# Kernel optimization log

Hardware: AMD Instinct MI355X
Metric: run time of the kernel (lower is better)

Reference implementation:

```python
import jax, jax.numpy as jnp
import numpy as np

N, E, F_IN, H, G, C = 50000, 600000, 128, 128, 500, 10


def _lin(k, fi, fo):
    # Glorot-ish scaled init for a [fi, fo] weight
    return (jax.random.normal(k, (fi, fo), jnp.float32) / np.float32(np.sqrt(fi)))


def setup_inputs() -> dict:
    key = jax.random.key(0)
    ks = jax.random.split(key, 16)
    x = jax.random.normal(ks[0], (N, F_IN), jnp.float32)
    edge_index = jax.random.randint(ks[1], (2, E), 0, N, dtype=jnp.int32)
    batch = jnp.sort(jax.random.randint(ks[2], (N,), 0, G, dtype=jnp.int32))
    return {
        "x": x, "edge_index": edge_index, "batch": batch,
        # SAGEConv i: out = mean_aggr @ Wl + bl + x @ Wr  (PyG default: mean aggr, root weight, bias on lin_l)
        "Wl1": _lin(ks[3], F_IN, H), "bl1": jnp.zeros((H,), jnp.float32), "Wr1": _lin(ks[4], F_IN, H),
        "Wl2": _lin(ks[5], H, H),    "bl2": jnp.zeros((H,), jnp.float32), "Wr2": _lin(ks[6], H, H),
        "Wl3": _lin(ks[7], H, H),    "bl3": jnp.zeros((H,), jnp.float32), "Wr3": _lin(ks[8], H, H),
        "W4": _lin(ks[9], H, 64), "b4": jnp.zeros((64,), jnp.float32),
        "W5": _lin(ks[10], 64, C), "b5": jnp.zeros((C,), jnp.float32),
    }


def _segment_mean(vals, ids, num_segments):
    s = jax.ops.segment_sum(vals, ids, num_segments=num_segments)
    cnt = jax.ops.segment_sum(jnp.ones((vals.shape[0], 1), vals.dtype), ids, num_segments=num_segments)
    return s / jnp.maximum(cnt, 1.0)


def _sage_conv(x, src, dst, Wl, bl, Wr):
    # gather source features along edges, mean-aggregate at destinations
    aggr = _segment_mean(x[src], dst, N)  # [N, F]
    return aggr @ Wl + bl + x @ Wr


def reference(x, edge_index, batch, Wl1, bl1, Wr1, Wl2, bl2, Wr2, Wl3, bl3, Wr3, W4, b4, W5, b5):
    src, dst = edge_index[0], edge_index[1]
    h = jax.nn.relu(_sage_conv(x, src, dst, Wl1, bl1, Wr1))
    h = jax.nn.relu(_sage_conv(h, src, dst, Wl2, bl2, Wr2))
    h = jax.nn.relu(_sage_conv(h, src, dst, Wl3, bl3, Wr3))
    g = _segment_mean(h, batch, G)          # global mean pool -> [G, H]
    g = jax.nn.relu(g @ W4 + b4)
    return jax.nn.log_softmax(g @ W5 + b5, axis=-1)
```

## Files before the change

### kernel.cpp

```cpp
#include <hip/hip_runtime.h>
#include <hip/hip_bf16.h>
#include <math.h>

#define FH 128

typedef __attribute__((ext_vector_type(8))) short short8v;
typedef __attribute__((ext_vector_type(4))) float float4v;
typedef unsigned short ushort_t;
typedef unsigned int   uint32;

__device__ __forceinline__ ushort_t f2bf(float f) {
    uint32 u = __builtin_bit_cast(uint32, f);
    u += 0x7fffu + ((u >> 16) & 1u);
    return (ushort_t)(u >> 16);
}
__device__ __forceinline__ float bf_lo(uint32 w) { return __builtin_bit_cast(float, w << 16); }
__device__ __forceinline__ float bf_hi(uint32 w) { return __builtin_bit_cast(float, w & 0xffff0000u); }
__device__ __forceinline__ uint32 pack2(float lo, float hi) {
    return (uint32)f2bf(lo) | ((uint32)f2bf(hi) << 16);
}

__global__ __launch_bounds__(256) void zero_kernel(int* __restrict__ p, int n) {
    int i = (blockIdx.x * 256 + threadIdx.x) * 4;
    if (i + 3 < n) {
        *(int4*)(p + i) = make_int4(0, 0, 0, 0);
    } else {
        for (int j = i; j < n; ++j) p[j] = 0;
    }
}

__device__ __forceinline__ void pack_one(const float* __restrict__ Wl,
                                         const float* __restrict__ Wr,
                                         ushort_t* __restrict__ Bp, int t) {
    int k = t >> 7, n = t & 127;
    float v = (k < FH) ? Wl[k * FH + n] : Wr[(k - FH) * FH + n];
    int nt = n >> 4, kt = k >> 5;
    int lane = (n & 15) + (((k >> 3) & 3) << 4);
    int j = k & 7;
    Bp[(((nt * 8 + kt) * 64) + lane) * 8 + j] = f2bf(v);
}

__global__ __launch_bounds__(256) void fused_prep_kernel(
        const float* __restrict__ x, ushort_t* __restrict__ xb, size_t n, int cvtBlocks,
        const float* __restrict__ Wl1, const float* __restrict__ Wr1, ushort_t* __restrict__ Bp1,
        const float* __restrict__ Wl2, const float* __restrict__ Wr2, ushort_t* __restrict__ Bp2,
        const float* __restrict__ Wl3, const float* __restrict__ Wr3, ushort_t* __restrict__ Bp3,
        const int* __restrict__ dst, int* __restrict__ deg, int E, int degBlocks,
        const int* __restrict__ batch, int* __restrict__ gstart, int N, int G) {
    int b = blockIdx.x;
    if (b < cvtBlocks) {
        size_t base = ((size_t)b * 256 + threadIdx.x) * 8;
        if (base >= n) return;
        const float4 a = *(const float4*)(x + base);
        const float4 c = *(const float4*)(x + base + 4);
        ushort_t o[8] = {f2bf(a.x), f2bf(a.y), f2bf(a.z), f2bf(a.w),
                         f2bf(c.x), f2bf(c.y), f2bf(c.z), f2bf(c.w)};
        *(uint4*)(xb + base) = *(const uint4*)o;
        return;
    }
    b -= cvtBlocks;
    if (b < 384) {
        int which = b >> 7;
        int t = (b & 127) * 256 + threadIdx.x;
        if (which == 0)      pack_one(Wl1, Wr1, Bp1, t);
        else if (which == 1) pack_one(Wl2, Wr2, Bp2, t);
        else                 pack_one(Wl3, Wr3, Bp3, t);
        return;
    }
    b -= 384;
    if (b < degBlocks) {
        int e = b * 256 + threadIdx.x;
        if (e < E) atomicAdd(&deg[dst[e]], 1);
        return;
    }
    b -= degBlocks;
    {
        int g = b * 256 + threadIdx.x;
        if (g > G) return;
        int lo = 0, hi = N;
        while (lo < hi) {
            int mid = (lo + hi) >> 1;
            if (batch[mid] < g) lo = mid + 1; else hi = mid;
        }
        gstart[g] = lo;
    }
}

__global__ __launch_bounds__(256) void scan1_kernel(const int* __restrict__ deg,
                                                    int* __restrict__ rowptr,
                                                    int* __restrict__ blockSums, int N) {
    __shared__ int lds[256];
    const int base = blockIdx.x * 1024;
    const int t = threadIdx.x;
    int v[4]; int sum = 0;
    #pragma unroll
    for (int j = 0; j < 4; ++j) {
        int idx = base + t * 4 + j;
        v[j] = (idx < N) ? deg[idx] : 0;
        sum += v[j];
    }
    lds[t] = sum; __syncthreads();
    for (int off = 1; off < 256; off <<= 1) {
        int val = lds[t];
        int add = (t >= off) ? lds[t - off] : 0;
        __syncthreads();
        lds[t] = val + add;
        __syncthreads();
    }
    int run = (t > 0) ? lds[t - 1] : 0;
    #pragma unroll
    for (int j = 0; j < 4; ++j) {
        int idx = base + t * 4 + j;
        if (idx < N) rowptr[idx] = run;
        run += v[j];
    }
    if (t == 255) blockSums[blockIdx.x] = lds[255];
}

__global__ __launch_bounds__(256) void scan3_kernel(int* __restrict__ rowptr,
                                                    int* __restrict__ pos,
                                                    const int* __restrict__ blockSums,
                                                    int N, int nb) {
    __shared__ int sAdd, sTot;
    if (threadIdx.x < 64) {
        const int lane = threadIdx.x;
        const int bid = blockIdx.x;
        int pre = 0, tot = 0;
        for (int i = lane; i < nb; i += 64) {
            const int v = blockSums[i];
            tot += v;
            if (i < bid) pre += v;
        }
        #pragma unroll
        for (int off = 1; off < 64; off <<= 1) {
            pre += __shfl_xor(pre, off);
            tot += __shfl_xor(tot, off);
        }
        if (lane == 0) { sAdd = pre; sTot = tot; }
    }
    __syncthreads();
    const int add = sAdd;
    const int base = blockIdx.x * 1024;
    #pragma unroll
    for (int j = 0; j < 4; ++j) {
        int idx = base + threadIdx.x * 4 + j;
        if (idx < N) {
            int v = rowptr[idx] + add;
            rowptr[idx] = v;
            pos[idx] = v;
        }
    }
    if (blockIdx.x == (unsigned)(nb - 1) && threadIdx.x == 0) rowptr[N] = sTot;
}

__global__ __launch_bounds__(256) void fill_csr_kernel(const int* __restrict__ src,
                                                       const int* __restrict__ dst,
                                                       int* __restrict__ pos,
                                                       int* __restrict__ csr, int E) {
    int e = blockIdx.x * 256 + threadIdx.x;
    if (e >= E) return;
    int idx = atomicAdd(&pos[dst[e]], 1);
    csr[idx] = src[e];
}

__global__ __launch_bounds__(256) void pull_mean_kernel(const ushort_t* __restrict__ x,
                                                        const int* __restrict__ rowptr,
                                                        const int* __restrict__ csr,
                                                        ushort_t* __restrict__ aggr, int N) {
    const int v = (blockIdx.x * 256 + threadIdx.x) >> 6;
    if (v >= N) return;
    const int lane = threadIdx.x & 63;
    const int grp  = lane >> 4;
    const int li   = lane & 15;
    const int beg = rowptr[v], end = rowptr[v + 1];
    const uint4* xp = (const uint4*)x + li;

    const uint4 z = {0u, 0u, 0u, 0u};
    uint4 w0 = z, w1 = z, w2 = z, w3 = z;
    const int i0 = beg + grp;
    if (i0 < end)      w0 = xp[(size_t)csr[i0] * 16];
    if (i0 + 4 < end)  w1 = xp[(size_t)csr[i0 + 4] * 16];
    if (i0 + 8 < end)  w2 = xp[(size_t)csr[i0 + 8] * 16];
    if (i0 + 12 < end) w3 = xp[(size_t)csr[i0 + 12] * 16];

    float a0 = (bf_lo(w0.x) + bf_lo(w1.x)) + (bf_lo(w2.x) + bf_lo(w3.x));
    float a1 = (bf_hi(w0.x) + bf_hi(w1.x)) + (bf_hi(w2.x) + bf_hi(w3.x));
    float a2 = (bf_lo(w0.y) + bf_lo(w1.y)) + (bf_lo(w2.y) + bf_lo(w3.y));
    float a3 = (bf_hi(w0.y) + bf_hi(w1.y)) + (bf_hi(w2.y) + bf_hi(w3.y));
    float a4 = (bf_lo(w0.z) + bf_lo(w1.z)) + (bf_lo(w2.z) + bf_lo(w3.z));
    float a5 = (bf_hi(w0.z) + bf_hi(w1.z)) + (bf_hi(w2.z) + bf_hi(w3.z));
    float a6 = (bf_lo(w0.w) + bf_lo(w1.w)) + (bf_lo(w2.w) + bf_lo(w3.w));
    float a7 = (bf_hi(w0.w) + bf_hi(w1.w)) + (bf_hi(w2.w) + bf_hi(w3.w));

    for (int i = beg + 16 + grp; i < end; i += 4) {
        const uint4 w = xp[(size_t)csr[i] * 16];
        a0 += bf_lo(w.x); a1 += bf_hi(w.x); a2 += bf_lo(w.y); a3 += bf_hi(w.y);
        a4 += bf_lo(w.z); a5 += bf_hi(w.z); a6 += bf_lo(w.w); a7 += bf_hi(w.w);
    }

    a0 += __shfl_xor(a0, 16); a1 += __shfl_xor(a1, 16);
    a2 += __shfl_xor(a2, 16); a3 += __shfl_xor(a3, 16);
    a4 += __shfl_xor(a4, 16); a5 += __shfl_xor(a5, 16);
    a6 += __shfl_xor(a6, 16); a7 += __shfl_xor(a7, 16);
    a0 += __shfl_xor(a0, 32); a1 += __shfl_xor(a1, 32);
    a2 += __shfl_xor(a2, 32); a3 += __shfl_xor(a3, 32);
    a4 += __shfl_xor(a4, 32); a5 += __shfl_xor(a5, 32);
    a6 += __shfl_xor(a6, 32); a7 += __shfl_xor(a7, 32);

    if (grp == 0) {
        const float inv = 1.0f / (float)max(end - beg, 1);
        uint4 o;
        o.x = pack2(a0 * inv, a1 * inv);
        o.y = pack2(a2 * inv, a3 * inv);
        o.z = pack2(a4 * inv, a5 * inv);
        o.w = pack2(a6 * inv, a7 * inv);
        ((uint4*)aggr)[(size_t)v * 16 + li] = o;
    }
}

#define SO_STRIDE 136
__global__ __launch_bounds__(256) void sage_mfma_kernel(const ushort_t* __restrict__ xin,
                                                        const ushort_t* __restrict__ aggr,
                                                        const ushort_t* __restrict__ Bp,
                                                        const float* __restrict__ bl,
                                                        ushort_t* __restrict__ out, int M) {
    __shared__ ushort_t sB[16384];
    const int tid = threadIdx.x;
    const int wave = tid >> 6;
    const int lane = tid & 63;
    const int grp  = lane >> 4;
    const int li   = lane & 15;
    const int rowBase = (blockIdx.x * 4 + wave) * 16;
    const int arow = min(rowBase + li, M - 1);

    short8v afrag[8];
    #pragma unroll
    for (int kt = 0; kt < 4; ++kt)
        afrag[kt] = *(const short8v*)(aggr + (size_t)arow * FH + kt * 32 + grp * 8);
    #pragma unroll
    for (int kt = 0; kt < 4; ++kt)
        afrag[4 + kt] = *(const short8v*)(xin + (size_t)arow * FH + kt * 32 + grp * 8);

    float4v acc[8];
    #pragma unroll
    for (int ch = 0; ch < 2; ++ch) {
        if (ch) __syncthreads();
        {
            const uint4* s = (const uint4*)Bp + ch * 2048;
            uint4* d = (uint4*)sB;
            #pragma unroll
            for (int i = 0; i < 8; ++i)
                d[tid + 256 * i] = s[tid + 256 * i];
        }
        __syncthreads();
        #pragma unroll
        for (int ntl = 0; ntl < 4; ++ntl) {
            const int nt = ch * 4 + ntl;
            acc[nt] = (float4v){0.f, 0.f, 0.f, 0.f};
            #pragma unroll
            for (int kt = 0; kt < 8; ++kt) {
                const short8v b = *(const short8v*)(sB + (((ntl * 8 + kt) * 64) + lane) * 8);
                acc[nt] = __builtin_amdgcn_mfma_f32_16x16x32_bf16(afrag[kt], b, acc[nt], 0, 0, 0);
            }
        }
    }

    __syncthreads();

    ushort_t* so = sB + wave * (16 * SO_STRIDE);
    #pragma unroll
    for (int nt = 0; nt < 8; ++nt) {
        const float bias = bl[nt * 16 + li];
        #pragma unroll
        for (int r = 0; r < 4; ++r)
            so[(grp * 4 + r) * SO_STRIDE + nt * 16 + li] = f2bf(fmaxf(acc[nt][r] + bias, 0.f));
    }
    #pragma unroll
    for (int t = 0; t < 4; ++t) {
        const int idx = lane + 64 * t;
        const int r  = idx >> 4;
        const int ch = idx & 15;
        const int row = rowBase + r;
        if (row < M) {
            const uint4 val = *(const uint4*)(so + r * SO_STRIDE + ch * 8);
            *(uint4*)(out + (size_t)row * FH + ch * 8) = val;
        }
    }
}

__global__ __launch_bounds__(256) void head_kernel(const ushort_t* __restrict__ h,
                                                   const int* __restrict__ gstart,
                                                   const float* __restrict__ W4,
                                                   const float* __restrict__ b4,
                                                   const float* __restrict__ W5,
                                                   const float* __restrict__ b5,
                                                   float* __restrict__ out, int G) {
    __shared__ float sred[4][FH];
    __shared__ float sg2[64];
    __shared__ float sl[10];
    __shared__ float slse;
    const int g = blockIdx.x;
    const int t = threadIdx.x;
    const int wave = t >> 6, lane = t & 63;
    const int beg = gstart[g], end = gstart[g + 1];

    const uint32* hp = (const uint32*)h + lane;
    float a0 = 0.f, a1 = 0.f;
    for (int i = beg + wave; i < end; i += 4) {
        const uint32 w = hp[(size_t)i * 64];
        a0 += bf_lo(w); a1 += bf_hi(w);
    }
    sred[wave][lane * 2]     = a0;
    sred[wave][lane * 2 + 1] = a1;
    __syncthreads();
    if (t < FH) {
        const float s = sred[0][t] + sred[1][t] + sred[2][t] + sred[3][t];
        sred[0][t] = s / (float)max(end - beg, 1);
    }
    __syncthreads();
    if (t < 64) {
        float acc = b4[t];
        #pragma unroll 4
        for (int k = 0; k < FH; ++k)
            acc += sred[0][k] * W4[k * 64 + t];
        sg2[t] = fmaxf(acc, 0.f);
    }
    __syncthreads();
    if (t < 10) {
        float acc = b5[t];
        #pragma unroll 4
        for (int k = 0; k < 64; ++k)
            acc += sg2[k] * W5[k * 10 + t];
        sl[t] = acc;
    }
    __syncthreads();
    if (t == 0) {
        float m = sl[0];
        #pragma unroll
        for (int j = 1; j < 10; ++j) m = fmaxf(m, sl[j]);
        float s = 0.f;
        #pragma unroll
        for (int j = 0; j < 10; ++j) s += expf(sl[j] - m);
        slse = m + logf(s);
    }
    __syncthreads();
    if (t < 10) out[g * 10 + t] = sl[t] - slse;
}

extern "C" void kernel_launch(void* const* d_in, const int* in_sizes, int n_in,
                              void* d_out, int out_size, void* d_ws, size_t ws_size,
                              hipStream_t stream) {
    const float* x     = (const float*)d_in[0];
    const int*   ei    = (const int*)d_in[1];
    const int*   batch = (const int*)d_in[2];
    const float* Wl1 = (const float*)d_in[3];
    const float* bl1 = (const float*)d_in[4];
    const float* Wr1 = (const float*)d_in[5];
    const float* Wl2 = (const float*)d_in[6];
    const float* bl2 = (const float*)d_in[7];
    const float* Wr2 = (const float*)d_in[8];
    const float* Wl3 = (const float*)d_in[9];
    const float* bl3 = (const float*)d_in[10];
    const float* Wr3 = (const float*)d_in[11];
    const float* W4  = (const float*)d_in[12];
    const float* b4  = (const float*)d_in[13];
    const float* W5  = (const float*)d_in[14];
    const float* b5  = (const float*)d_in[15];
    float* out = (float*)d_out;

    const int N = in_sizes[0] / FH;
    const int E = in_sizes[1] / 2;
    const int G = out_size / 10;
    const int* src = ei;
    const int* dst = ei + E;

    char* p = (char*)d_ws;
    auto take = [&](size_t bytes) { char* q = p; p += (bytes + 255) & ~(size_t)255; return q; };
    ushort_t* xb    = (ushort_t*)take((size_t)N * FH * 2);
    ushort_t* h     = (ushort_t*)take((size_t)N * FH * 2);
    ushort_t* aggrb = (ushort_t*)take((size_t)N * FH * 2);
    int* deg        = (int*)take((size_t)N * 4);
    int* rowptr     = (int*)take((size_t)(N + 1) * 4);
    int* pos        = (int*)take((size_t)N * 4);
    int* csr        = (int*)take((size_t)E * 4);
    int* blockSums  = (int*)take(256 * 4);
    ushort_t* Bp1   = (ushort_t*)take(256 * FH * 2);
    ushort_t* Bp2   = (ushort_t*)take(256 * FH * 2);
    ushort_t* Bp3   = (ushort_t*)take(256 * FH * 2);
    int* gstart     = (int*)take((size_t)(G + 1) * 4);

    const int nb = (N + 1023) / 1024;

    zero_kernel<<<(N / 4 + 255) / 256, 256, 0, stream>>>(deg, N);

    const int cvtBlocks = (int)(((size_t)N * FH / 8 + 255) / 256);
    const int degBlocks = (E + 255) / 256;
    const int gbBlocks  = (G + 1 + 255) / 256;
    fused_prep_kernel<<<cvtBlocks + 384 + degBlocks + gbBlocks, 256, 0, stream>>>(
        x, xb, (size_t)N * FH, cvtBlocks,
        Wl1, Wr1, Bp1, Wl2, Wr2, Bp2, Wl3, Wr3, Bp3,
        dst, deg, E, degBlocks,
        batch, gstart, N, G);

    scan1_kernel<<<nb, 256, 0, stream>>>(deg, rowptr, blockSums, N);
    scan3_kernel<<<nb, 256, 0, stream>>>(rowptr, pos, blockSums, N, nb);
    fill_csr_kernel<<<(E + 255) / 256, 256, 0, stream>>>(src, dst, pos, csr, E);

    const int pullGrid = (N * 64 + 255) / 256;
    const int gemmGrid = (N + 63) / 64;

    pull_mean_kernel<<<pullGrid, 256, 0, stream>>>(xb, rowptr, csr, aggrb, N);
    sage_mfma_kernel<<<gemmGrid, 256, 0, stream>>>(xb, aggrb, Bp1, bl1, h, N);

    pull_mean_kernel<<<pullGrid, 256, 0, stream>>>(h, rowptr, csr, aggrb, N);
    sage_mfma_kernel<<<gemmGrid, 256, 0, stream>>>(h, aggrb, Bp2, bl2, h, N);

    pull_mean_kernel<<<pullGrid, 256, 0, stream>>>(h, rowptr, csr, aggrb, N);
    sage_mfma_kernel<<<gemmGrid, 256, 0, stream>>>(h, aggrb, Bp3, bl3, h, N);

    head_kernel<<<G, 256, 0, stream>>>(h, gstart, W4, b4, W5, b5, out, G);
}
```

Measured before the change: 221.4 us.

## Split GEMM tile across waves, read weights from global, widen gather prefetch

The SAGE GEMM kernel no longer stages the full 32KB weight block into shared memory. Each wave now computes half the output columns for a 16-row tile and reads B fragments straight from global/L2, which shrinks LDS use and removes block barriers so occupancy can rise. The pull-mean kernel issues six independent neighbour loads up front instead of four, giving more memory-level parallelism. The hidden buffer is now double-buffered (hA/hB), so a GEMM never overwrites the same array it reads. The cost is redundant A-fragment loads per wave pair and more global traffic for B, which relies on cache hits.

After: 228.7 us. 3.3% more time.

```diff
diff --git a/kernel.cpp b/kernel.cpp
--- a/kernel.cpp
+++ b/kernel.cpp
@@ -176,23 +176,25 @@
     const uint4* xp = (const uint4*)x + li;
 
     const uint4 z = {0u, 0u, 0u, 0u};
-    uint4 w0 = z, w1 = z, w2 = z, w3 = z;
+    uint4 w0 = z, w1 = z, w2 = z, w3 = z, w4 = z, w5 = z;
     const int i0 = beg + grp;
     if (i0 < end)      w0 = xp[(size_t)csr[i0] * 16];
     if (i0 + 4 < end)  w1 = xp[(size_t)csr[i0 + 4] * 16];
     if (i0 + 8 < end)  w2 = xp[(size_t)csr[i0 + 8] * 16];
     if (i0 + 12 < end) w3 = xp[(size_t)csr[i0 + 12] * 16];
-
-    float a0 = (bf_lo(w0.x) + bf_lo(w1.x)) + (bf_lo(w2.x) + bf_lo(w3.x));
-    float a1 = (bf_hi(w0.x) + bf_hi(w1.x)) + (bf_hi(w2.x) + bf_hi(w3.x));
-    float a2 = (bf_lo(w0.y) + bf_lo(w1.y)) + (bf_lo(w2.y) + bf_lo(w3.y));
-    float a3 = (bf_hi(w0.y) + bf_hi(w1.y)) + (bf_hi(w2.y) + bf_hi(w3.y));
-    float a4 = (bf_lo(w0.z) + bf_lo(w1.z)) + (bf_lo(w2.z) + bf_lo(w3.z));
-    float a5 = (bf_hi(w0.z) + bf_hi(w1.z)) + (bf_hi(w2.z) + bf_hi(w3.z));
-    float a6 = (bf_lo(w0.w) + bf_lo(w1.w)) + (bf_lo(w2.w) + bf_lo(w3.w));
-    float a7 = (bf_hi(w0.w) + bf_hi(w1.w)) + (bf_hi(w2.w) + bf_hi(w3.w));
-
-    for (int i = beg + 16 + grp; i < end; i += 4) {
+    if (i0 + 16 < end) w4 = xp[(size_t)csr[i0 + 16] * 16];
+    if (i0 + 20 < end) w5 = xp[(size_t)csr[i0 + 20] * 16];
+
+    float a0 = (bf_lo(w0.x) + bf_lo(w1.x)) + (bf_lo(w2.x) + bf_lo(w3.x)) + (bf_lo(w4.x) + bf_lo(w5.x));
+    float a1 = (bf_hi(w0.x) + bf_hi(w1.x)) + (bf_hi(w2.x) + bf_hi(w3.x)) + (bf_hi(w4.x) + bf_hi(w5.x));
+    float a2 = (bf_lo(w0.y) + bf_lo(w1.y)) + (bf_lo(w2.y) + bf_lo(w3.y)) + (bf_lo(w4.y) + bf_lo(w5.y));
+    float a3 = (bf_hi(w0.y) + bf_hi(w1.y)) + (bf_hi(w2.y) + bf_hi(w3.y)) + (bf_hi(w4.y) + bf_hi(w5.y));
+    float a4 = (bf_lo(w0.z) + bf_lo(w1.z)) + (bf_lo(w2.z) + bf_lo(w3.z)) + (bf_lo(w4.z) + bf_lo(w5.z));
+    float a5 = (bf_hi(w0.z) + bf_hi(w1.z)) + (bf_hi(w2.z) + bf_hi(w3.z)) + (bf_hi(w4.z) + bf_hi(w5.z));
+    float a6 = (bf_lo(w0.w) + bf_lo(w1.w)) + (bf_lo(w2.w) + bf_lo(w3.w)) + (bf_lo(w4.w) + bf_lo(w5.w));
+    float a7 = (bf_hi(w0.w) + bf_hi(w1.w)) + (bf_hi(w2.w) + bf_hi(w3.w)) + (bf_hi(w4.w) + bf_hi(w5.w));
+
+    for (int i = beg + 24 + grp; i < end; i += 4) {
         const uint4 w = xp[(size_t)csr[i] * 16];
         a0 += bf_lo(w.x); a1 += bf_hi(w.x); a2 += bf_lo(w.y); a3 += bf_hi(w.y);
         a4 += bf_lo(w.z); a5 += bf_hi(w.z); a6 += bf_lo(w.w); a7 += bf_hi(w.w);
@@ -218,19 +220,21 @@
     }
 }
 
-#define SO_STRIDE 136
 __global__ __launch_bounds__(256) void sage_mfma_kernel(const ushort_t* __restrict__ xin,
                                                         const ushort_t* __restrict__ aggr,
                                                         const ushort_t* __restrict__ Bp,
                                                         const float* __restrict__ bl,
                                                         ushort_t* __restrict__ out, int M) {
-    __shared__ ushort_t sB[16384];
-    const int tid = threadIdx.x;
+    __shared__ ushort_t so[4][16 * 72];
+    const int tid  = threadIdx.x;
     const int wave = tid >> 6;
     const int lane = tid & 63;
     const int grp  = lane >> 4;
     const int li   = lane & 15;
-    const int rowBase = (blockIdx.x * 4 + wave) * 16;
+    const int rowHalf = wave >> 1;
+    const int ntHalf  = wave & 1;
+    const int rowBase = blockIdx.x * 32 + rowHalf * 16;
+    if (rowBase >= M) return;
     const int arow = min(rowBase + li, M - 1);
 
     short8v afrag[8];
@@ -241,49 +245,36 @@
     for (int kt = 0; kt < 4; ++kt)
         afrag[4 + kt] = *(const short8v*)(xin + (size_t)arow * FH + kt * 32 + grp * 8);
 
-    float4v acc[8];
-    #pragma unroll
-    for (int ch = 0; ch < 2; ++ch) {
-        if (ch) __syncthreads();
-        {
-            const uint4* s = (const uint4*)Bp + ch * 2048;
-            uint4* d = (uint4*)sB;
-            #pragma unroll
-            for (int i = 0; i < 8; ++i)
-                d[tid + 256 * i] = s[tid + 256 * i];
-        }
-        __syncthreads();
+    const ushort_t* BpW = Bp + (size_t)ntHalf * 4 * 8 * 64 * 8;
+    float4v acc[4];
+    #pragma unroll
+    for (int ntl = 0; ntl < 4; ++ntl) {
+        acc[ntl] = (float4v){0.f, 0.f, 0.f, 0.f};
         #pragma unroll
-        for (int ntl = 0; ntl < 4; ++ntl) {
-            const int nt = ch * 4 + ntl;
-            acc[nt] = (float4v){0.f, 0.f, 0.f, 0.f};
-            #pragma unroll
-            for (int kt = 0; kt < 8; ++kt) {
-                const short8v b = *(const short8v*)(sB + (((ntl * 8 + kt) * 64) + lane) * 8);
-                acc[nt] = __builtin_amdgcn_mfma_f32_16x16x32_bf16(afrag[kt], b, acc[nt], 0, 0, 0);
-            }
-        }
-    }
-
-    __syncthreads();
-
-    ushort_t* so = sB + wave * (16 * SO_STRIDE);
-    #pragma unroll
-    for (int nt = 0; nt < 8; ++nt) {
+        for (int kt = 0; kt < 8; ++kt) {
+            const short8v b = *(const short8v*)(BpW + (((ntl * 8 + kt) * 64) + lane) * 8);
+            acc[ntl] = __builtin_amdgcn_mfma_f32_16x16x32_bf16(afrag[kt], b, acc[ntl], 0, 0, 0);
+        }
+    }
+
+    ushort_t* s = so[wave];
+    #pragma unroll
+    for (int ntl = 0; ntl < 4; ++ntl) {
+        const int nt = ntHalf * 4 + ntl;
         const float bias = bl[nt * 16 + li];
         #pragma unroll
         for (int r = 0; r < 4; ++r)
-            so[(grp * 4 + r) * SO_STRIDE + nt * 16 + li] = f2bf(fmaxf(acc[nt][r] + bias, 0.f));
-    }
-    #pragma unroll
-    for (int t = 0; t < 4; ++t) {
+            s[(grp * 4 + r) * 72 + ntl * 16 + li] = f2bf(fmaxf(acc[ntl][r] + bias, 0.f));
+    }
+    #pragma unroll
+    for (int t = 0; t < 2; ++t) {
         const int idx = lane + 64 * t;
-        const int r  = idx >> 4;
-        const int ch = idx & 15;
+        const int r   = idx >> 3;
+        const int ch  = idx & 7;
         const int row = rowBase + r;
         if (row < M) {
-            const uint4 val = *(const uint4*)(so + r * SO_STRIDE + ch * 8);
-            *(uint4*)(out + (size_t)row * FH + ch * 8) = val;
+            const uint4 val = *(const uint4*)(s + r * 72 + ch * 8);
+            *(uint4*)(out + (size_t)row * FH + ntHalf * 64 + ch * 8) = val;
         }
     }
 }
@@ -377,7 +368,8 @@
     char* p = (char*)d_ws;
     auto take = [&](size_t bytes) { char* q = p; p += (bytes + 255) & ~(size_t)255; return q; };
     ushort_t* xb    = (ushort_t*)take((size_t)N * FH * 2);
-    ushort_t* h     = (ushort_t*)take((size_t)N * FH * 2);
+    ushort_t* hA    = (ushort_t*)take((size_t)N * FH * 2);
+    ushort_t* hB    = (ushort_t*)take((size_t)N * FH * 2);
     ushort_t* aggrb = (ushort_t*)take((size_t)N * FH * 2);
     int* deg        = (int*)take((size_t)N * 4);
     int* rowptr     = (int*)take((size_t)(N + 1) * 4);
@@ -407,16 +399,16 @@
     fill_csr_kernel<<<(E + 255) / 256, 256, 0, stream>>>(src, dst, pos, csr, E);
 
     const int pullGrid = (N * 64 + 255) / 256;
-    const int gemmGrid = (N + 63) / 64;
+    const int gemmGrid = (N + 31) / 32;
 
     pull_mean_kernel<<<pullGrid, 256, 0, stream>>>(xb, rowptr, csr, aggrb, N);
-    sage_mfma_kernel<<<gemmGrid, 256, 0, stream>>>(xb, aggrb, Bp1, bl1, h, N);
-
-    pull_mean_kernel<<<pullGrid, 256, 0, stream>>>(h, rowptr, csr, aggrb, N);
-    sage_mfma_kernel<<<gemmGrid, 256, 0, stream>>>(h, aggrb, Bp2, bl2, h, N);
-
-    pull_mean_kernel<<<pullGrid, 256, 0, stream>>>(h, rowptr, csr, aggrb, N);
-    sage_mfma_kernel<<<gemmGrid, 256, 0, stream>>>(h, aggrb, Bp3, bl3, h, N);
-
-    head_kernel<<<G, 256, 0, stream>>>(h, gstart, W4, b4, W5, b5, out, G);
-}
+    sage_mfma_kernel<<<gemmGrid, 256, 0, stream>>>(xb, aggrb, Bp1, bl1, hA, N);
+
+    pull_mean_kernel<<<pullGrid, 256, 0, stream>>>(hA, rowptr, csr, aggrb, N);
+    sage_mfma_kernel<<<gemmGrid, 256, 0, stream>>>(hA, aggrb, Bp2, bl2, hB, N);
+
+    pull_mean_kernel<<<pullGrid, 256, 0, stream>>>(hB, rowptr, csr, aggrb, N);
+    sage_mfma_kernel<<<gemmGrid, 256, 0, stream>>>(hB, aggrb, Bp3, bl3, hA, N);
+
+    head_kernel<<<G, 256, 0, stream>>>(hA, gstart, W4, b4, W5, b5, out, G);
+}
```
